# Kernel tuning notes

Measured on AMD Instinct MI355X. Metric: run time of the kernel, lower is better.

Reference implementation:

```python
import jax, jax.numpy as jnp
import numpy as np

N_NODES = 100000
N_EDGES = 1250000
IN_F = 128
OUT_F = 64


def setup_inputs() -> dict:
    key = jax.random.key(0)
    k1, k2, k3, k4 = jax.random.split(key, 4)
    x = jax.random.normal(k1, (N_NODES, IN_F), dtype=jnp.float32)
    weight = jax.random.normal(k2, (IN_F, OUT_F), dtype=jnp.float32) * (6.0 / (IN_F + OUT_F)) ** 0.5
    bias = jnp.zeros((OUT_F,), dtype=jnp.float32)
    edge_weight = jax.random.uniform(k3, (N_EDGES,), dtype=jnp.float32)
    edge_index = jax.random.randint(k4, (2, N_EDGES), 0, N_NODES, dtype=jnp.int64)
    return {"x": x, "weight": weight, "bias": bias, "edge_weight": edge_weight, "edge_index": edge_index}


def reference(x, weight, bias, edge_weight, edge_index):
    # Linear transform: [N, in] @ [in, out] -> [N, out]
    h = x @ weight
    src, dst = edge_index[0], edge_index[1]
    # Gather source node features, scale by edge weight: [E, out]
    x_j = h[src] * edge_weight[:, None]
    n = x.shape[0]
    # scatter_add of messages and edge counts per destination node
    out = jax.ops.segment_sum(x_j, dst, num_segments=n)
    count = jax.ops.segment_sum(jnp.ones_like(edge_weight), dst, num_segments=n)
    out = out / jnp.clip(count, 1.0)[:, None]  # scatter_mean with min-count 1
    out = out + bias
    return jax.nn.relu(out)
```

## Files before the change

kernel.cpp:

```cpp
#include <hip/hip_runtime.h>

#define N_NODES 100000
#define N_EDGES 1250000
#define IN_F 128
#define OUT_F 64

#define GR 32
__global__ __launch_bounds__(256) void gemm2_k(const float* __restrict__ x,
                                               const float* __restrict__ w,
                                               float* __restrict__ h) {
    __shared__ float wlds[IN_F * OUT_F];
    __shared__ float xlds[GR * IN_F];
    const int t = threadIdx.x;

    const float4* w4 = (const float4*)w;
    float4* wl4 = (float4*)wlds;
    #pragma unroll
    for (int i = t; i < IN_F * OUT_F / 4; i += 256) wl4[i] = w4[i];

    const long row0 = (long)blockIdx.x * GR;
    const float4* x4 = (const float4*)(x + row0 * IN_F);
    float4* xl4 = (float4*)xlds;
    #pragma unroll
    for (int i = t; i < GR * IN_F / 4; i += 256) xl4[i] = x4[i];

    __syncthreads();

    const int col = t & 63;
    const int wv  = t >> 6;
    float acc[8];
    #pragma unroll
    for (int r = 0; r < 8; ++r) acc[r] = 0.f;

    #pragma unroll
    for (int k = 0; k < IN_F; k += 4) {
        const float w0 = wlds[(k + 0) * OUT_F + col];
        const float w1 = wlds[(k + 1) * OUT_F + col];
        const float w2 = wlds[(k + 2) * OUT_F + col];
        const float w3 = wlds[(k + 3) * OUT_F + col];
        #pragma unroll
        for (int r = 0; r < 8; ++r) {
            const float4 xv = *(const float4*)&xlds[(wv * 8 + r) * IN_F + k];
            acc[r] += xv.x * w0 + xv.y * w1 + xv.z * w2 + xv.w * w3;
        }
    }

    #pragma unroll
    for (int r = 0; r < 8; ++r)
        h[(row0 + wv * 8 + r) * OUT_F + col] = acc[r];
}

__global__ __launch_bounds__(256) void hist_k(const int* __restrict__ dst,
                                              int* __restrict__ cnt) {
    const int e = blockIdx.x * 256 + threadIdx.x;
    if (e >= N_EDGES) return;
    atomicAdd(&cnt[dst[e]], 1);
}

#define SCAN_B 1024
__global__ __launch_bounds__(256) void scan1_k(const int* __restrict__ cnt,
                                               int* __restrict__ start,
                                               int* __restrict__ bsum) {
    __shared__ int lds[256];
    const int t = threadIdx.x;
    const int base = blockIdx.x * SCAN_B + t * 4;
    int v0 = 0, v1 = 0, v2 = 0, v3 = 0;
    if (base + 0 < N_NODES) v0 = cnt[base + 0];
    if (base + 1 < N_NODES) v1 = cnt[base + 1];
    if (base + 2 < N_NODES) v2 = cnt[base + 2];
    if (base + 3 < N_NODES) v3 = cnt[base + 3];
    const int s = v0 + v1 + v2 + v3;
    lds[t] = s;
    __syncthreads();
    #pragma unroll
    for (int off = 1; off < 256; off <<= 1) {
        const int add = (t >= off) ? lds[t - off] : 0;
        __syncthreads();
        lds[t] += add;
        __syncthreads();
    }
    const int excl = lds[t] - s;
    if (base + 0 < N_NODES) start[base + 0] = excl;
    if (base + 1 < N_NODES) start[base + 1] = excl + v0;
    if (base + 2 < N_NODES) start[base + 2] = excl + v0 + v1;
    if (base + 3 < N_NODES) start[base + 3] = excl + v0 + v1 + v2;
    if (t == 255) bsum[blockIdx.x] = lds[t];
}

#define NSCAN_BLOCKS ((N_NODES + SCAN_B - 1) / SCAN_B)
__global__ __launch_bounds__(128) void scan2_k(int* __restrict__ bsum) {
    __shared__ int lds[128];
    const int t = threadIdx.x;
    const int v = (t < NSCAN_BLOCKS) ? bsum[t] : 0;
    lds[t] = v;
    __syncthreads();
    #pragma unroll
    for (int off = 1; off < 128; off <<= 1) {
        const int add = (t >= off) ? lds[t - off] : 0;
        __syncthreads();
        lds[t] += add;
        __syncthreads();
    }
    if (t < NSCAN_BLOCKS) bsum[t] = lds[t] - v;
}

__global__ __launch_bounds__(256) void scan3_k(int* __restrict__ start,
                                               int* __restrict__ pos,
                                               const int* __restrict__ bsum) {
    const int i = blockIdx.x * 256 + threadIdx.x;
    if (i >= N_NODES) return;
    const int v = start[i] + bsum[i / SCAN_B];
    start[i] = v;
    pos[i] = v;
}

__global__ __launch_bounds__(256) void bucket_k(const int* __restrict__ src,
                                                const int* __restrict__ dst,
                                                const float* __restrict__ ew,
                                                int* __restrict__ pos,
                                                uint2* __restrict__ pairs) {
    const int e = blockIdx.x * 256 + threadIdx.x;
    if (e >= N_EDGES) return;
    const int d = dst[e];
    const int p = atomicAdd(&pos[d], 1);
    pairs[p] = make_uint2((unsigned)src[e], __float_as_uint(ew[e]));
}

__global__ __launch_bounds__(256) void accum_k(const float* __restrict__ h,
                                               const uint2* __restrict__ pairs,
                                               const int* __restrict__ start,
                                               const int* __restrict__ cnt,
                                               const float* __restrict__ bias,
                                               float* __restrict__ out) {
    const int node = blockIdx.x * 4 + (threadIdx.x >> 6);
    const int lane = threadIdx.x & 63;
    const int q  = lane >> 4;
    const int ql = lane & 15;
    const int s0 = start[node];
    const int c  = cnt[node];

    float4 acc = make_float4(0.f, 0.f, 0.f, 0.f);
    for (int i = s0 + q; i < s0 + c; i += 4) {
        const uint2 pr = pairs[i];
        const float wgt = __uint_as_float(pr.y);
        const float4 hv = ((const float4*)(h + (size_t)pr.x * OUT_F))[ql];
        acc.x += hv.x * wgt;
        acc.y += hv.y * wgt;
        acc.z += hv.z * wgt;
        acc.w += hv.w * wgt;
    }

    #pragma unroll
    for (int m = 16; m <= 32; m <<= 1) {
        acc.x += __shfl_xor(acc.x, m, 64);
        acc.y += __shfl_xor(acc.y, m, 64);
        acc.z += __shfl_xor(acc.z, m, 64);
        acc.w += __shfl_xor(acc.w, m, 64);
    }

    if (q == 0) {
        float cf = (float)c;
        if (cf < 1.f) cf = 1.f;
        const float inv = 1.0f / cf;
        const float4 b = ((const float4*)bias)[ql];
        float4 v;
        v.x = acc.x * inv + b.x;
        v.y = acc.y * inv + b.y;
        v.z = acc.z * inv + b.z;
        v.w = acc.w * inv + b.w;
        v.x = v.x > 0.f ? v.x : 0.f;
        v.y = v.y > 0.f ? v.y : 0.f;
        v.z = v.z > 0.f ? v.z : 0.f;
        v.w = v.w > 0.f ? v.w : 0.f;
        ((float4*)(out + (size_t)node * OUT_F))[ql] = v;
    }
}

__global__ __launch_bounds__(256) void scatter_k(const float* __restrict__ h,
                                                 const float* __restrict__ ew,
                                                 const int* __restrict__ src,
                                                 const int* __restrict__ dst,
                                                 float* __restrict__ out,
                                                 float* __restrict__ cnt) {
    const int e = blockIdx.x * 4 + (threadIdx.x >> 6);
    if (e >= N_EDGES) return;
    const int lane = threadIdx.x & 63;
    const int   s = src[e];
    const int   d = dst[e];
    const float w = ew[e];
    const float v = h[(long)s * OUT_F + lane] * w;
    atomicAdd(&out[(long)d * OUT_F + lane], v);
    if (lane == 0) atomicAdd(&cnt[d], 1.0f);
}

__global__ __launch_bounds__(256) void final_k(float* __restrict__ out,
                                               const float* __restrict__ cnt,
                                               const float* __restrict__ bias) {
    const int tid = blockIdx.x * 256 + threadIdx.x;
    if (tid >= N_NODES * OUT_F) return;
    const int n = tid >> 6;
    const int f = tid & 63;
    float c = cnt[n];
    if (c < 1.0f) c = 1.0f;
    float v = out[tid] / c + bias[f];
    out[tid] = v > 0.0f ? v : 0.0f;
}

extern "C" void kernel_launch(void* const* d_in, const int* in_sizes, int n_in,
                              void* d_out, int out_size, void* d_ws, size_t ws_size,
                              hipStream_t stream) {
    const float* x    = (const float*)d_in[0];
    const float* w    = (const float*)d_in[1];
    const float* bias = (const float*)d_in[2];
    const float* ew   = (const float*)d_in[3];
    const int*   ei   = (const int*)d_in[4];

    float* out = (float*)d_out;
    const int* src = ei;
    const int* dst = ei + N_EDGES;

    char* ws = (char*)d_ws;
    float* h     = (float*)(ws);
    int*   cnt   = (int*)(ws + 25600000);
    int*   start = (int*)(ws + 26000000);
    int*   pos   = (int*)(ws + 26400000);
    int*   bsum  = (int*)(ws + 26800000);
    uint2* pairs = (uint2*)(ws + 26801024);
    const size_t WS_NEEDED = 26801024 + (size_t)N_EDGES * sizeof(uint2);

    gemm2_k<<<N_NODES / GR, 256, 0, stream>>>(x, w, h);

    if (ws_size >= WS_NEEDED) {
        hipMemsetAsync(cnt, 0, N_NODES * sizeof(int), stream);
        hist_k<<<(N_EDGES + 255) / 256, 256, 0, stream>>>(dst, cnt);
        scan1_k<<<NSCAN_BLOCKS, 256, 0, stream>>>(cnt, start, bsum);
        scan2_k<<<1, 128, 0, stream>>>(bsum);
        scan3_k<<<(N_NODES + 255) / 256, 256, 0, stream>>>(start, pos, bsum);
        bucket_k<<<(N_EDGES + 255) / 256, 256, 0, stream>>>(src, dst, ew, pos, pairs);
        accum_k<<<N_NODES / 4, 256, 0, stream>>>(h, pairs, start, cnt, bias, out);
    } else {
        float* fcnt = (float*)cnt;
        hipMemsetAsync(out, 0, (size_t)N_NODES * OUT_F * sizeof(float), stream);
        hipMemsetAsync(fcnt, 0, N_NODES * sizeof(float), stream);
        scatter_k<<<(N_EDGES + 3) / 4, 256, 0, stream>>>(h, ew, src, dst, out, fcnt);
        final_k<<<(N_NODES * OUT_F + 255) / 256, 256, 0, stream>>>(out, fcnt, bias);
    }
}
```

Before: 334.5 us.

## Bucket edges by 128-node groups and accumulate in LDS tiles with atomics

```diff
diff --git a/kernel.cpp b/kernel.cpp
--- a/kernel.cpp
+++ b/kernel.cpp
@@ -104,70 +104,81 @@
     if (t < NSCAN_BLOCKS) bsum[t] = lds[t] - v;
 }
 
+#define BNBITS 7
+#define BNODES 128
+#define NBUCK ((N_NODES + BNODES - 1) / BNODES)
 __global__ __launch_bounds__(256) void scan3_k(int* __restrict__ start,
-                                               int* __restrict__ pos,
+                                               int* __restrict__ bpos,
                                                const int* __restrict__ bsum) {
     const int i = blockIdx.x * 256 + threadIdx.x;
     if (i >= N_NODES) return;
     const int v = start[i] + bsum[i / SCAN_B];
     start[i] = v;
-    pos[i] = v;
-}
-
-__global__ __launch_bounds__(256) void bucket_k(const int* __restrict__ src,
-                                                const int* __restrict__ dst,
-                                                const float* __restrict__ ew,
-                                                int* __restrict__ pos,
-                                                uint2* __restrict__ pairs) {
+    if ((i & (BNODES - 1)) == 0) bpos[i >> BNBITS] = v;
+}
+
+__global__ __launch_bounds__(256) void bscatter_k(const int* __restrict__ src,
+                                                  const int* __restrict__ dst,
+                                                  const float* __restrict__ ew,
+                                                  int* __restrict__ bpos,
+                                                  uint2* __restrict__ recs) {
     const int e = blockIdx.x * 256 + threadIdx.x;
     if (e >= N_EDGES) return;
     const int d = dst[e];
-    const int p = atomicAdd(&pos[d], 1);
-    pairs[p] = make_uint2((unsigned)src[e], __float_as_uint(ew[e]));
-}
-
-__global__ __launch_bounds__(256) void accum_k(const float* __restrict__ h,
-                                               const uint2* __restrict__ pairs,
-                                               const int* __restrict__ start,
-                                               const int* __restrict__ cnt,
-                                               const float* __restrict__ bias,
-                                               float* __restrict__ out) {
-    const int node = blockIdx.x * 4 + (threadIdx.x >> 6);
-    const int lane = threadIdx.x & 63;
+    const int p = atomicAdd(&bpos[d >> BNBITS], 1);
+    const unsigned pack = (unsigned)src[e] | ((unsigned)(d & (BNODES - 1)) << 17);
+    recs[p] = make_uint2(pack, __float_as_uint(ew[e]));
+}
+
+__global__ __launch_bounds__(256) void accum_lds_k(const float* __restrict__ h,
+                                                   const uint2* __restrict__ recs,
+                                                   const int* __restrict__ start,
+                                                   const int* __restrict__ cnt,
+                                                   const float* __restrict__ bias,
+                                                   float* __restrict__ out) {
+    __shared__ float tile[BNODES][OUT_F];
+    const int b = blockIdx.x;
+    const int t = threadIdx.x;
+
+    float4* tz = (float4*)&tile[0][0];
+    #pragma unroll
+    for (int i = t; i < BNODES * OUT_F / 4; i += 256)
+        tz[i] = make_float4(0.f, 0.f, 0.f, 0.f);
+    __syncthreads();
+
+    const int s0 = start[b * BNODES];
+    const int e1 = (b == NBUCK - 1) ? N_EDGES : start[(b + 1) * BNODES];
+
+    const int lane = t & 63;
+    const int wv = t >> 6;
     const int q  = lane >> 4;
     const int ql = lane & 15;
-    const int s0 = start[node];
-    const int c  = cnt[node];
-
-    float4 acc = make_float4(0.f, 0.f, 0.f, 0.f);
-    for (int i = s0 + q; i < s0 + c; i += 4) {
-        const uint2 pr = pairs[i];
-        const float wgt = __uint_as_float(pr.y);
-        const float4 hv = ((const float4*)(h + (size_t)pr.x * OUT_F))[ql];
-        acc.x += hv.x * wgt;
-        acc.y += hv.y * wgt;
-        acc.z += hv.z * wgt;
-        acc.w += hv.w * wgt;
-    }
-
-    #pragma unroll
-    for (int m = 16; m <= 32; m <<= 1) {
-        acc.x += __shfl_xor(acc.x, m, 64);
-        acc.y += __shfl_xor(acc.y, m, 64);
-        acc.z += __shfl_xor(acc.z, m, 64);
-        acc.w += __shfl_xor(acc.w, m, 64);
-    }
-
-    if (q == 0) {
-        float cf = (float)c;
-        if (cf < 1.f) cf = 1.f;
-        const float inv = 1.0f / cf;
-        const float4 b = ((const float4*)bias)[ql];
-        float4 v;
-        v.x = acc.x * inv + b.x;
-        v.y = acc.y * inv + b.y;
-        v.z = acc.z * inv + b.z;
-        v.w = acc.w * inv + b.w;
+
+    for (int i = s0 + wv * 4 + q; i < e1; i += 16) {
+        const uint2 r = recs[i];
+        const unsigned sn = r.x & 0x1FFFFu;
+        const int dl = (int)(r.x >> 17);
+        const float w = __uint_as_float(r.y);
+        const float4 hv = ((const float4*)(h + (size_t)sn * OUT_F))[ql];
+        atomicAdd(&tile[dl][ql * 4 + 0], hv.x * w);
+        atomicAdd(&tile[dl][ql * 4 + 1], hv.y * w);
+        atomicAdd(&tile[dl][ql * 4 + 2], hv.z * w);
+        atomicAdd(&tile[dl][ql * 4 + 3], hv.w * w);
+    }
+    __syncthreads();
+
+    const float4 bb = ((const float4*)bias)[ql];
+    for (int r0 = wv * 4 + q; r0 < BNODES; r0 += 16) {
+        const int node = b * BNODES + r0;
+        if (node >= N_NODES) break;
+        float c = (float)cnt[node];
+        if (c < 1.f) c = 1.f;
+        const float inv = 1.0f / c;
+        float4 v = *(float4*)&tile[r0][ql * 4];
+        v.x = v.x * inv + bb.x;
+        v.y = v.y * inv + bb.y;
+        v.z = v.z * inv + bb.z;
+        v.w = v.w * inv + bb.w;
         v.x = v.x > 0.f ? v.x : 0.f;
         v.y = v.y > 0.f ? v.y : 0.f;
         v.z = v.z > 0.f ? v.z : 0.f;
@@ -223,9 +234,9 @@
     float* h     = (float*)(ws);
     int*   cnt   = (int*)(ws + 25600000);
     int*   start = (int*)(ws + 26000000);
-    int*   pos   = (int*)(ws + 26400000);
+    int*   bpos  = (int*)(ws + 26400000);
     int*   bsum  = (int*)(ws + 26800000);
-    uint2* pairs = (uint2*)(ws + 26801024);
+    uint2* recs  = (uint2*)(ws + 26801024);
     const size_t WS_NEEDED = 26801024 + (size_t)N_EDGES * sizeof(uint2);
 
     gemm2_k<<<N_NODES / GR, 256, 0, stream>>>(x, w, h);
@@ -235,9 +246,9 @@
         hist_k<<<(N_EDGES + 255) / 256, 256, 0, stream>>>(dst, cnt);
         scan1_k<<<NSCAN_BLOCKS, 256, 0, stream>>>(cnt, start, bsum);
         scan2_k<<<1, 128, 0, stream>>>(bsum);
-        scan3_k<<<(N_NODES + 255) / 256, 256, 0, stream>>>(start, pos, bsum);
-        bucket_k<<<(N_EDGES + 255) / 256, 256, 0, stream>>>(src, dst, ew, pos, pairs);
-        accum_k<<<N_NODES / 4, 256, 0, stream>>>(h, pairs, start, cnt, bias, out);
+        scan3_k<<<(N_NODES + 255) / 256, 256, 0, stream>>>(start, bpos, bsum);
+        bscatter_k<<<(N_EDGES + 255) / 256, 256, 0, stream>>>(src, dst, ew, bpos, recs);
+        accum_lds_k<<<NBUCK, 256, 0, stream>>>(h, recs, start, cnt, bias, out);
     } else {
         float* fcnt = (float*)cnt;
         hipMemsetAsync(out, 0, (size_t)N_NODES * OUT_F * sizeof(float), stream);
```

Measured after the change: 1.017 ms. +204.0%, slower.

## Retile dense GEMM with 4x4 register blocking and swizzled x tile

Applied to the files above, without the earlier changes.

```diff
diff --git a/kernel.cpp b/kernel.cpp
--- a/kernel.cpp
+++ b/kernel.cpp
@@ -5,49 +5,67 @@
 #define IN_F 128
 #define OUT_F 64
 
-#define GR 32
-__global__ __launch_bounds__(256) void gemm2_k(const float* __restrict__ x,
+#define TM 64
+__global__ __launch_bounds__(256) void gemm3_k(const float* __restrict__ x,
                                                const float* __restrict__ w,
                                                float* __restrict__ h) {
     __shared__ float wlds[IN_F * OUT_F];
-    __shared__ float xlds[GR * IN_F];
+    __shared__ float xlds[TM * IN_F];
     const int t = threadIdx.x;
-
-    const float4* w4 = (const float4*)w;
+    const int row0 = blockIdx.x * TM;
+
+    const float4* w4p = (const float4*)w;
     float4* wl4 = (float4*)wlds;
     #pragma unroll
-    for (int i = t; i < IN_F * OUT_F / 4; i += 256) wl4[i] = w4[i];
-
-    const long row0 = (long)blockIdx.x * GR;
-    const float4* x4 = (const float4*)(x + row0 * IN_F);
-    float4* xl4 = (float4*)xlds;
-    #pragma unroll
-    for (int i = t; i < GR * IN_F / 4; i += 256) xl4[i] = x4[i];
-
+    for (int i = 0; i < 8; ++i) wl4[t + i * 256] = w4p[t + i * 256];
+
+    #pragma unroll
+    for (int i = 0; i < 8; ++i) {
+        const int idx = t + i * 256;
+        const int r   = idx >> 5;
+        const int k4  = idx & 31;
+        float4 v = make_float4(0.f, 0.f, 0.f, 0.f);
+        if (row0 + r < N_NODES)
+            v = ((const float4*)(x + (size_t)(row0 + r) * IN_F))[k4];
+        const int k4s = (k4 + r) & 31;
+        *(float4*)&xlds[r * IN_F + k4s * 4] = v;
+    }
     __syncthreads();
 
-    const int col = t & 63;
-    const int wv  = t >> 6;
-    float acc[8];
-    #pragma unroll
-    for (int r = 0; r < 8; ++r) acc[r] = 0.f;
-
-    #pragma unroll
-    for (int k = 0; k < IN_F; k += 4) {
-        const float w0 = wlds[(k + 0) * OUT_F + col];
-        const float w1 = wlds[(k + 1) * OUT_F + col];
-        const float w2 = wlds[(k + 2) * OUT_F + col];
-        const float w3 = wlds[(k + 3) * OUT_F + col];
+    const int colg = t & 15;
+    const int rowg = t >> 4;
+    float acc[4][4];
+    #pragma unroll
+    for (int i = 0; i < 4; ++i)
         #pragma unroll
-        for (int r = 0; r < 8; ++r) {
-            const float4 xv = *(const float4*)&xlds[(wv * 8 + r) * IN_F + k];
-            acc[r] += xv.x * w0 + xv.y * w1 + xv.z * w2 + xv.w * w3;
+        for (int j = 0; j < 4; ++j) acc[i][j] = 0.f;
+
+    #pragma unroll 8
+    for (int k4 = 0; k4 < 32; ++k4) {
+        float4 wv[4];
+        #pragma unroll
+        for (int kk = 0; kk < 4; ++kk)
+            wv[kk] = *(const float4*)&wlds[(k4 * 4 + kk) * OUT_F + colg * 4];
+        #pragma unroll
+        for (int i = 0; i < 4; ++i) {
+            const int r = rowg * 4 + i;
+            const int k4s = (k4 + r) & 31;
+            const float4 xv = *(const float4*)&xlds[r * IN_F + k4s * 4];
+            acc[i][0] += xv.x * wv[0].x + xv.y * wv[1].x + xv.z * wv[2].x + xv.w * wv[3].x;
+            acc[i][1] += xv.x * wv[0].y + xv.y * wv[1].y + xv.z * wv[2].y + xv.w * wv[3].y;
+            acc[i][2] += xv.x * wv[0].z + xv.y * wv[1].z + xv.z * wv[2].z + xv.w * wv[3].z;
+            acc[i][3] += xv.x * wv[0].w + xv.y * wv[1].w + xv.z * wv[2].w + xv.w * wv[3].w;
         }
     }
 
     #pragma unroll
-    for (int r = 0; r < 8; ++r)
-        h[(row0 + wv * 8 + r) * OUT_F + col] = acc[r];
+    for (int i = 0; i < 4; ++i) {
+        const int r = row0 + rowg * 4 + i;
+        if (r < N_NODES) {
+            float4 v = make_float4(acc[i][0], acc[i][1], acc[i][2], acc[i][3]);
+            *(float4*)&h[(size_t)r * OUT_F + colg * 4] = v;
+        }
+    }
 }
 
 __global__ __launch_bounds__(256) void hist_k(const int* __restrict__ dst,
@@ -228,7 +246,7 @@
     uint2* pairs = (uint2*)(ws + 26801024);
     const size_t WS_NEEDED = 26801024 + (size_t)N_EDGES * sizeof(uint2);
 
-    gemm2_k<<<N_NODES / GR, 256, 0, stream>>>(x, w, h);
+    gemm3_k<<<(N_NODES + TM - 1) / TM, 256, 0, stream>>>(x, w, h);
 
     if (ws_size >= WS_NEEDED) {
         hipMemsetAsync(cnt, 0, N_NODES * sizeof(int), stream);
```

Result: faster. 327.9 us (-2.0%).
